# Kernel tuning notes

Measured on AMD Instinct MI355X. Metric: run time of the kernel, lower is better.

The kernel has to match this reference:

```python
import jax, jax.numpy as jnp
import numpy as np

DIM = 256
NH = 4
HD = DIM // NH
RR = 8
EPS_BN = 1e-5


def dwconv(x, w, b):
    # depthwise conv, stride 1, SAME padding (odd kernel, pad=k//2)
    out = jax.lax.conv_general_dilated(
        x, w, window_strides=(1, 1), padding='SAME',
        feature_group_count=x.shape[1],
        dimension_numbers=('NCHW', 'OIHW', 'NCHW'))
    return out + b[None, :, None, None]


def conv1x1(x, w, b):
    # w: [out_c, in_c]
    return jnp.einsum('bchw,oc->bohw', x, w) + b[None, :, None, None]


def bn_eval(x, g, be, m, v):
    inv = g / jnp.sqrt(v + EPS_BN)
    return x * inv[None, :, None, None] + (be - m * inv)[None, :, None, None]


def l2norm(x):
    n = jnp.sqrt(jnp.sum(x * x, axis=-1, keepdims=True))
    return x / jnp.maximum(n, 1e-12)


def setup_inputs() -> dict:
    key = jax.random.key(0)
    ks = jax.random.split(key, 32)
    d = {}
    d['x1'] = jax.random.normal(ks[0], (8, DIM, 64, 64), jnp.float32)
    d['x2'] = jax.random.normal(ks[1], (8, DIM, 64, 64), jnp.float32)
    # multi-scale depthwise convs k=3,5,7
    for i, k in enumerate([3, 5, 7]):
        d[f'ms_w{k}'] = jax.random.normal(ks[2 + i], (DIM, 1, k, k), jnp.float32) * (1.0 / k)
        d[f'ms_b{k}'] = jax.random.normal(ks[5 + i], (DIM,), jnp.float32) * 0.02
    # qkv 1x1 conv + BN params for each stream
    for s, off in [(1, 8), (2, 16)]:
        d[f'qkv{s}_w'] = jax.random.normal(ks[off], (3 * DIM, DIM), jnp.float32) * (DIM ** -0.5)
        d[f'qkv{s}_b'] = jnp.zeros((3 * DIM,), jnp.float32)
        d[f'bn{s}_g'] = 1.0 + 0.1 * jax.random.normal(ks[off + 1], (3 * DIM,), jnp.float32)
        d[f'bn{s}_b'] = 0.1 * jax.random.normal(ks[off + 2], (3 * DIM,), jnp.float32)
        d[f'bn{s}_m'] = 0.1 * jax.random.normal(ks[off + 3], (3 * DIM,), jnp.float32)
        d[f'bn{s}_v'] = jax.random.uniform(ks[off + 4], (3 * DIM,), jnp.float32, 0.5, 1.5)
    # SE channel attention (shared module)
    d['ca_w1'] = jax.random.normal(ks[24], (DIM // RR, DIM), jnp.float32) * (DIM ** -0.5)
    d['ca_b1'] = jnp.zeros((DIM // RR,), jnp.float32)
    d['ca_w2'] = jax.random.normal(ks[25], (DIM, DIM // RR), jnp.float32) * ((DIM // RR) ** -0.5)
    d['ca_b2'] = jnp.zeros((DIM,), jnp.float32)
    # output projections
    d['po1_w'] = jax.random.normal(ks[26], (DIM, DIM), jnp.float32) * (DIM ** -0.5)
    d['po1_b'] = jnp.zeros((DIM,), jnp.float32)
    d['po2_w'] = jax.random.normal(ks[27], (DIM, DIM), jnp.float32) * (DIM ** -0.5)
    d['po2_b'] = jnp.zeros((DIM,), jnp.float32)
    return d


def _scfa(x1, x2, ms_w3, ms_b3, ms_w5, ms_b5, ms_w7, ms_b7,
          qkv1_w, qkv1_b, bn1_g, bn1_b, bn1_m, bn1_v,
          qkv2_w, qkv2_b, bn2_g, bn2_b, bn2_m, bn2_v,
          ca_w1, ca_b1, ca_w2, ca_b2, po1_w, po1_b, po2_w, po2_b):
    b, c, h, w = x1.shape
    temp = HD ** -0.5

    def multi_scale(x):
        return (dwconv(x, ms_w3, ms_b3) + dwconv(x, ms_w5, ms_b5) + dwconv(x, ms_w7, ms_b7)) / 3.0

    x1f = multi_scale(x1)
    x2f = multi_scale(x2)

    qkv1 = jax.nn.gelu(bn_eval(conv1x1(x1f, qkv1_w, qkv1_b), bn1_g, bn1_b, bn1_m, bn1_v), approximate=False)
    qkv2 = jax.nn.gelu(bn_eval(conv1x1(x2f, qkv2_w, qkv2_b), bn2_g, bn2_b, bn2_m, bn2_v), approximate=False)

    def split_heads(t):
        q, k, v = jnp.split(t, 3, axis=1)
        f = lambda z: z.reshape(b, NH, HD, h * w)
        return f(q), f(k), f(v)

    x1_q, x1_k, x1_v = split_heads(qkv1)
    x2_q, x2_k, x2_v = split_heads(qkv2)

    q1, k2 = l2norm(x1_q), l2norm(x2_k)
    q2, k1 = l2norm(x2_q), l2norm(x1_k)

    attn1 = jax.nn.softmax(jnp.einsum('bhcn,bhdn->bhcd', q1, k2) * temp, axis=-1)
    attn2 = jax.nn.softmax(jnp.einsum('bhcn,bhdn->bhcd', q2, k1) * temp, axis=-1)

    x1_out = jnp.einsum('bhcd,bhdn->bhcn', attn1, x1_v).reshape(b, c, h, w)
    x2_out = jnp.einsum('bhcd,bhdn->bhcn', attn2, x2_v).reshape(b, c, h, w)

    def se_gate(x):
        p = x.mean(axis=(2, 3))  # [b, c]
        y = jax.nn.relu(jnp.einsum('bc,rc->br', p, ca_w1) + ca_b1)
        y = jax.nn.sigmoid(jnp.einsum('br,cr->bc', y, ca_w2) + ca_b2)
        return y[:, :, None, None]

    x1_out = x1_out * se_gate(x1_out)
    x2_out = x2_out * se_gate(x2_out)

    x1_out = conv1x1(x1_out, po1_w, po1_b) + x1
    x2_out = conv1x1(x2_out, po2_w, po2_b) + x2
    return x1_out, x2_out


def reference(x1, x2, ms_w3, ms_b3, ms_w5, ms_b5, ms_w7, ms_b7,
              qkv1_w, qkv1_b, bn1_g, bn1_b, bn1_m, bn1_v,
              qkv2_w, qkv2_b, bn2_g, bn2_b, bn2_m, bn2_v,
              ca_w1, ca_b1, ca_w2, ca_b2, po1_w, po1_b, po2_w, po2_b):
    return _scfa(x1, x2, ms_w3, ms_b3, ms_w5, ms_b5, ms_w7, ms_b7,
                 qkv1_w, qkv1_b, bn1_g, bn1_b, bn1_m, bn1_v,
                 qkv2_w, qkv2_b, bn2_g, bn2_b, bn2_m, bn2_v,
                 ca_w1, ca_b1, ca_w2, ca_b2, po1_w, po1_b, po2_w, po2_b)
```

## Files before the change

### kernel.cpp

```cpp
#include <hip/hip_runtime.h>
#include <hip/hip_bf16.h>


#define NPIX 4096

typedef __attribute__((ext_vector_type(8))) short bfrag;
typedef __attribute__((ext_vector_type(4))) float f4acc;

#define GLDS16(g, l) __builtin_amdgcn_global_load_lds( \
    (const __attribute__((address_space(1))) unsigned int*)(g), \
    (__attribute__((address_space(3))) unsigned int*)(l), 16, 0, 0)

__device__ __forceinline__ float bf2f(unsigned short h) {
  return __uint_as_float(((unsigned)h) << 16);
}
__device__ __forceinline__ unsigned short f2bf(float f) {
  unsigned u = __float_as_uint(f);
  unsigned r = (u + 0x7FFFu + ((u >> 16) & 1u)) >> 16;
  return (unsigned short)r;
}
__device__ __forceinline__ float gelu_f(float x) {
  float z = x * (1.5957691216f + 0.0713548163f * x * x);
  return x / (1.0f + __expf(-z));
}

__global__ __launch_bounds__(256) void prep_kernel(
    const float* __restrict__ w3, const float* __restrict__ b3,
    const float* __restrict__ w5, const float* __restrict__ b5,
    const float* __restrict__ w7, const float* __restrict__ b7,
    const float* __restrict__ qb1, const float* __restrict__ g1,
    const float* __restrict__ be1, const float* __restrict__ m1,
    const float* __restrict__ v1,
    const float* __restrict__ qb2, const float* __restrict__ g2,
    const float* __restrict__ be2, const float* __restrict__ m2,
    const float* __restrict__ v2,
    float* __restrict__ weff, float* __restrict__ beff,
    float* __restrict__ alpha, float* __restrict__ beta)
{
  const int c = threadIdx.x;
  for (int ky = 0; ky < 7; ++ky)
    for (int kx = 0; kx < 7; ++kx) {
      float w = w7[c * 49 + ky * 7 + kx];
      if (ky >= 1 && ky <= 5 && kx >= 1 && kx <= 5)
        w += w5[c * 25 + (ky - 1) * 5 + (kx - 1)];
      if (ky >= 2 && ky <= 4 && kx >= 2 && kx <= 4)
        w += w3[c * 9 + (ky - 2) * 3 + (kx - 2)];
      weff[c * 49 + ky * 7 + kx] = w * (1.0f / 3.0f);
    }
  beff[c] = (b3[c] + b5[c] + b7[c]) * (1.0f / 3.0f);
  for (int o = c; o < 768; o += 256) {
    float inv1 = g1[o] / sqrtf(v1[o] + 1e-5f);
    alpha[o] = inv1;
    beta[o]  = qb1[o] * inv1 + be1[o] - m1[o] * inv1;
    float inv2 = g2[o] / sqrtf(v2[o] + 1e-5f);
    alpha[768 + o] = inv2;
    beta[768 + o]  = qb2[o] * inv2 + be2[o] - m2[o] * inv2;
  }
}

__global__ __launch_bounds__(256) void convert_w(
    const float* __restrict__ s1, const float* __restrict__ s2,
    unsigned short* __restrict__ d1, unsigned short* __restrict__ d2)
{
  int idx = blockIdx.x * 256 + threadIdx.x;
  d1[idx] = f2bf(s1[idx]);
  d2[idx] = f2bf(s2[idx]);
}

__global__ __launch_bounds__(256) void ms_conv(
    const float* __restrict__ x1, const float* __restrict__ x2,
    const float* __restrict__ weff, const float* __restrict__ beff,
    unsigned short* __restrict__ xf0, unsigned short* __restrict__ xf1)
{
  __shared__ float tile[5888];
  const int bc2 = blockIdx.x;
  const int s = bc2 >> 11, bc = bc2 & 2047;
  const int c = bc & 255;
  const int tid = threadIdx.x;
  const float* src = (s ? x2 : x1) + (size_t)bc * NPIX;
  float wreg[49];
#pragma unroll
  for (int i = 0; i < 49; ++i) wreg[i] = weff[c * 49 + i];
  const float bias = beff[c];
  float4 vv[4];
#pragma unroll
  for (int k = 0; k < 4; ++k)
    vv[k] = *(const float4*)&src[(k * 256 + tid) * 4];
#pragma unroll
  for (int k = 0; k < 4; ++k) {
    const int idx = k * 256 + tid;
    const int row = (idx >> 4) + 3;
    const int col = 4 + (idx & 15) * 4;
    *(float4*)&tile[84 * row + ((row >> 3) & 1) * 8 + col] = vv[k];
  }
  const float4 zq = {0.0f, 0.0f, 0.0f, 0.0f};
  for (int idx = tid; idx < 306; idx += 256) {
    int row, col;
    if (idx < 114) {
      int r6 = idx / 19;
      col = (idx - r6 * 19) * 4;
      row = (r6 < 3) ? r6 : (r6 + 64);
    } else {
      int j = idx - 114;
      int r64 = j / 3, q = j - r64 * 3;
      row = 3 + r64;
      col = (q == 0) ? 0 : (64 + q * 4);
    }
    *(float4*)&tile[84 * row + ((row >> 3) & 1) * 8 + col] = zq;
  }
  __syncthreads();
  const int x0 = (tid & 15) * 4;
  const int y0 = (tid >> 4) * 4;
  float acc[4][4];
#pragma unroll
  for (int yo = 0; yo < 4; ++yo)
#pragma unroll
    for (int xo = 0; xo < 4; ++xo) acc[yo][xo] = bias;
#pragma unroll
  for (int r = 0; r < 10; ++r) {
    const int row = y0 + r;
    const int rb = 84 * row + ((row >> 3) & 1) * 8 + x0;
    float seg[12];
    *(float4*)&seg[0] = *(const float4*)&tile[rb];
    *(float4*)&seg[4] = *(const float4*)&tile[rb + 4];
    *(float4*)&seg[8] = *(const float4*)&tile[rb + 8];
    const int yolo = (r >= 6) ? (r - 6) : 0;
    const int yohi = (r < 3) ? r : 3;
#pragma unroll
    for (int yo = 0; yo < 4; ++yo) {
      if (yo < yolo || yo > yohi) continue;
      const int ky = r - yo;
#pragma unroll
      for (int kx = 0; kx < 7; ++kx) {
        const float w = wreg[ky * 7 + kx];
#pragma unroll
        for (int xo = 0; xo < 4; ++xo)
          acc[yo][xo] = fmaf(w, seg[1 + xo + kx], acc[yo][xo]);
      }
    }
  }
  unsigned short* dst = (s ? xf1 : xf0) + (size_t)bc * NPIX;
#pragma unroll
  for (int yo = 0; yo < 4; ++yo) {
    ushort4 u;
    u.x = f2bf(acc[yo][0]); u.y = f2bf(acc[yo][1]);
    u.z = f2bf(acc[yo][2]); u.w = f2bf(acc[yo][3]);
    *(ushort4*)&dst[(y0 + yo) * 64 + x0] = u;
  }
}

__global__ __launch_bounds__(256) void transpose_bf16(
    const unsigned short* __restrict__ s0, unsigned short* __restrict__ d0,
    const unsigned short* __restrict__ s1, unsigned short* __restrict__ d1,
    long sb, long db)
{
  __shared__ unsigned short T[64][72];
  const int n0 = blockIdx.x * 64, c0 = blockIdx.y * 64;
  const int z = blockIdx.z, st = z >> 3, b = z & 7;
  const unsigned short* src = st ? s1 : s0;
  unsigned short* dst = st ? d1 : d0;
  const int t = threadIdx.x;
  const int rhi = t >> 4, c4 = (t & 15) * 4;
#pragma unroll
  for (int rr = 0; rr < 4; ++rr) {
    int row = rr * 16 + rhi;
    ushort4 u = *(const ushort4*)&src[(size_t)b * sb + (size_t)(c0 + row) * NPIX + n0 + c4];
    T[row][c4 + 0] = u.x; T[row][c4 + 1] = u.y;
    T[row][c4 + 2] = u.z; T[row][c4 + 3] = u.w;
  }
  __syncthreads();
#pragma unroll
  for (int rr = 0; rr < 4; ++rr) {
    int nrow = rr * 16 + rhi;
    ushort4 u;
    u.x = T[c4 + 0][nrow]; u.y = T[c4 + 1][nrow];
    u.z = T[c4 + 2][nrow]; u.w = T[c4 + 3][nrow];
    *(ushort4*)&dst[(size_t)b * db + (size_t)(n0 + nrow) * 256 + c0 + c4] = u;
  }
}

__global__ __launch_bounds__(256) void qkv_gemm(
    const unsigned short* __restrict__ W1, const unsigned short* __restrict__ W2,
    const unsigned short* __restrict__ X0, const unsigned short* __restrict__ X1,
    const float* __restrict__ alpha, const float* __restrict__ beta,
    unsigned short* __restrict__ q1, unsigned short* __restrict__ q2,
    float* __restrict__ ns)
{
  __shared__ unsigned short As[128 * 64];
  __shared__ unsigned short Bs[256 * 64];
  const int n0 = blockIdx.x * 256, o0 = blockIdx.y * 128;
  const int z = blockIdx.z, s = z >> 3, b = z & 7;
  const unsigned short* Wb = s ? W2 : W1;
  const unsigned short* Xt = s ? X1 : X0;
  unsigned short* qkv = s ? q2 : q1;
  const float* al = alpha + s * 768;
  const float* be = beta + s * 768;
  float* normsq = ns + s * 4096;
  const int tid = threadIdx.x, w = tid >> 6, lane = tid & 63;
  const int wm = (w & 1) * 128;
  const int wn = (w >> 1) * 64;
  const int lrow8 = lane >> 3;
  const int lcolsw = ((lane & 7) ^ lrow8) * 8;
  const int fslot = lane & 7;
  f4acc acc[8][4] = {};
  auto stage = [&](int kc) {
#pragma unroll
    for (int j = 0; j < 4; ++j) {
      int i = w * 4 + j;
      GLDS16(Wb + (size_t)(o0 + i * 8 + lrow8) * 256 + kc + lcolsw, &As[i * 512]);
    }
#pragma unroll
    for (int j = 0; j < 8; ++j) {
      int i = w * 8 + j;
      GLDS16(Xt + (size_t)b * 1048576 + (size_t)(n0 + i * 8 + lrow8) * 256 + kc + lcolsw,
             &Bs[i * 512]);
    }
  };
  stage(0);
#pragma unroll
  for (int t = 0; t < 4; ++t) {
    __syncthreads();
#pragma unroll
    for (int ks = 0; ks < 2; ++ks) {
      const int slot = ((ks * 4 + (lane >> 4)) ^ fslot) * 8;
      bfrag a[8], bb[4];
#pragma unroll
      for (int mt = 0; mt < 8; ++mt)
        a[mt] = *(const bfrag*)&Bs[(wm + mt * 16 + (lane & 15)) * 64 + slot];
#pragma unroll
      for (int nt = 0; nt < 4; ++nt)
        bb[nt] = *(const bfrag*)&As[(wn + nt * 16 + (lane & 15)) * 64 + slot];
#pragma unroll
      for (int mt = 0; mt < 8; ++mt)
#pragma unroll
        for (int nt = 0; nt < 4; ++nt)
          acc[mt][nt] = __builtin_amdgcn_mfma_f32_16x16x32_bf16(a[mt], bb[nt], acc[mt][nt], 0, 0, 0);
    }
    if (t < 3) {
      __syncthreads();
      stage((t + 1) * 64);
    }
  }
#pragma unroll
  for (int nt = 0; nt < 4; ++nt) {
    const int o = o0 + wn + nt * 16 + (lane & 15);
    const float alv = al[o], bev = be[o];
    unsigned short* orow = qkv + ((size_t)b * 768 + o) * NPIX;
    float sq = 0.0f;
#pragma unroll
    for (int mt = 0; mt < 8; ++mt) {
      const int n = n0 + wm + mt * 16 + (lane >> 4) * 4;
      float v0 = gelu_f(acc[mt][nt][0] * alv + bev);
      float v1 = gelu_f(acc[mt][nt][1] * alv + bev);
      float v2 = gelu_f(acc[mt][nt][2] * alv + bev);
      float v3 = gelu_f(acc[mt][nt][3] * alv + bev);
      ushort4 u;
      u.x = f2bf(v0); u.y = f2bf(v1); u.z = f2bf(v2); u.w = f2bf(v3);
      *(ushort4*)&orow[n] = u;
      sq += v0 * v0 + v1 * v1 + v2 * v2 + v3 * v3;
    }
    if (o0 + wn + nt * 16 < 512) {
      sq += __shfl_xor(sq, 16);
      sq += __shfl_xor(sq, 32);
      if (lane < 16) atomicAdd(&normsq[b * 512 + o], sq);
    }
  }
}

__global__ __launch_bounds__(256) void spart_kernel(
    const unsigned short* __restrict__ qkv1, const unsigned short* __restrict__ qkv2,
    float* __restrict__ Sp0, float* __restrict__ Sp1)
{
  __shared__ unsigned short Qs[2][64 * 128];
  __shared__ unsigned short Ks[2][64 * 128];
  const int ck = blockIdx.x, h = blockIdx.y;
  const int z = blockIdx.z, s = z >> 3, b = z & 7;
  const unsigned short* qs = s ? qkv2 : qkv1;
  const unsigned short* kp = (s ? qkv1 : qkv2) + 256 * NPIX;
  float* Sp = s ? Sp1 : Sp0;
  const int tid = threadIdx.x, w = tid >> 6, lane = tid & 63;
  const int lrow16 = lane >> 4;
  const size_t qbase = ((size_t)b * 768 + h * 64) * NPIX;
  f4acc acc[4] = {};
  auto stage = [&](int buf, int it) {
    const int noff = ck * 512 + it * 128;
#pragma unroll
    for (int j = 0; j < 4; ++j) {
      int i = w * 4 + j;
      int row = i * 4 + lrow16;
      int colsw = ((lane & 15) ^ (row & 15)) * 8;
      GLDS16(qs + qbase + (size_t)row * NPIX + noff + colsw, &Qs[buf][i * 512]);
      GLDS16(kp + qbase + (size_t)row * NPIX + noff + colsw, &Ks[buf][i * 512]);
    }
  };
  stage(0, 0);
#pragma unroll
  for (int it = 0; it < 4; ++it) {
    const int cur = it & 1;
    if (it < 3) stage(cur ^ 1, it + 1);
    if (it < 3) asm volatile("s_waitcnt vmcnt(8)" ::: "memory");
    else        asm volatile("s_waitcnt vmcnt(0)" ::: "memory");
    __builtin_amdgcn_s_barrier();
#pragma unroll
    for (int kk = 0; kk < 4; ++kk) {
      const int slot = ((kk * 4 + (lane >> 4)) ^ (lane & 15)) * 8;
      bfrag bq = *(const bfrag*)&Qs[cur][(w * 16 + (lane & 15)) * 128 + slot];
#pragma unroll
      for (int mt = 0; mt < 4; ++mt) {
        bfrag ak = *(const bfrag*)&Ks[cur][(mt * 16 + (lane & 15)) * 128 + slot];
        acc[mt] = __builtin_amdgcn_mfma_f32_16x16x32_bf16(ak, bq, acc[mt], 0, 0, 0);
      }
    }
    __builtin_amdgcn_s_barrier();
  }
  float* dst = Sp + ((size_t)(ck * 32) + b * 4 + h) * 4096;
  const int c = w * 16 + (lane & 15);
#pragma unroll
  for (int mt = 0; mt < 4; ++mt)
    *(float4*)&dst[c * 64 + mt * 16 + (lane >> 4) * 4] = *(float4*)&acc[mt];
}

__global__ __launch_bounds__(256) void softattn(
    const float* __restrict__ Sp0, const float* __restrict__ Sp1,
    const float* __restrict__ ns,
    unsigned short* __restrict__ at0, unsigned short* __restrict__ at1)
{
  const int bh2 = blockIdx.x;
  const int s = bh2 >> 5, bh = bh2 & 31;
  const int b = bh >> 2, h = bh & 3;
  const float* Sp = s ? Sp1 : Sp0;
  const float* nsq = ns + s * 4096;
  const float* nsk = ns + (s ^ 1) * 4096;
  unsigned short* attn = s ? at1 : at0;
  const int wv = threadIdx.x >> 6, lane = threadIdx.x & 63;
  const float ikd = 1.0f / fmaxf(sqrtf(nsk[b * 512 + 256 + h * 64 + lane]), 1e-12f);
  for (int c = wv; c < 64; c += 4) {
    float sm = 0.0f;
#pragma unroll
    for (int ch = 0; ch < 8; ++ch)
      sm += Sp[((size_t)(ch * 32) + bh) * 4096 + c * 64 + lane];
    const float iq = 1.0f / fmaxf(sqrtf(nsq[b * 512 + h * 64 + c]), 1e-12f);
    float zv = sm * 0.125f * iq * ikd;
    float m = zv;
#pragma unroll
    for (int off = 32; off > 0; off >>= 1) m = fmaxf(m, __shfl_xor(m, off));
    float e = expf(zv - m);
    float sum = e;
#pragma unroll
    for (int off = 32; off > 0; off >>= 1) sum += __shfl_xor(sum, off);
    attn[(size_t)bh * 4096 + c * 64 + lane] = f2bf(e / sum);
  }
}

__global__ __launch_bounds__(256) void av_kernel(
    const unsigned short* __restrict__ vt0, const unsigned short* __restrict__ vt1,
    const unsigned short* __restrict__ at0, const unsigned short* __restrict__ at1,
    unsigned short* __restrict__ xo0, unsigned short* __restrict__ xo1,
    long db, float* __restrict__ pool)
{
  __shared__ unsigned short Vs[256 * 64];
  __shared__ unsigned short At[64 * 64];
  const int n0 = blockIdx.x * 256, h = blockIdx.y;
  const int z = blockIdx.z, s = z >> 3, b = z & 7;
  const unsigned short* vt = s ? vt1 : vt0;
  const unsigned short* attn = s ? at1 : at0;
  unsigned short* xout = s ? xo1 : xo0;
  float* pl = pool + s * 2048;
  const int tid = threadIdx.x, w = tid >> 6, lane = tid & 63;
  const int lrow8 = lane >> 3;
  const int lcolsw = ((lane & 7) ^ lrow8) * 8;
  const int bh = b * 4 + h;
#pragma unroll
  for (int j = 0; j < 8; ++j) {
    int i = w * 8 + j;
    GLDS16(vt + ((size_t)b * 1048576 + (size_t)(n0 + i * 8 + lrow8) * 256) + h * 64 + lcolsw,
           &Vs[i * 512]);
  }
#pragma unroll
  for (int j = 0; j < 2; ++j) {
    int i = w * 2 + j;
    GLDS16(attn + (size_t)bh * 4096 + (size_t)(i * 8 + lrow8) * 64 + lcolsw, &At[i * 512]);
  }
  __syncthreads();
  f4acc acc[4][4] = {};
#pragma unroll
  for (int ks = 0; ks < 2; ++ks) {
    const int slot = ((ks * 4 + (lane >> 4)) ^ (lane & 7)) * 8;
    bfrag a[4], bb[4];
#pragma unroll
    for (int mt = 0; mt < 4; ++mt)
      a[mt] = *(const bfrag*)&At[(mt * 16 + (lane & 15)) * 64 + slot];
#pragma unroll
    for (int nt = 0; nt < 4; ++nt)
      bb[nt] = *(const bfrag*)&Vs[(w * 64 + nt * 16 + (lane & 15)) * 64 + slot];
#pragma unroll
    for (int mt = 0; mt < 4; ++mt)
#pragma unroll
      for (int nt = 0; nt < 4; ++nt)
        acc[mt][nt] = __builtin_amdgcn_mfma_f32_16x16x32_bf16(a[mt], bb[nt], acc[mt][nt], 0, 0, 0);
  }
#pragma unroll
  for (int mt = 0; mt < 4; ++mt) {
    const int c = mt * 16 + (lane >> 4) * 4;
    float s0 = 0.0f, s1 = 0.0f, s2 = 0.0f, s3 = 0.0f;
#pragma unroll
    for (int nt = 0; nt < 4; ++nt) {
      const int np = n0 + w * 64 + nt * 16 + (lane & 15);
      ushort4 u;
      u.x = f2bf(acc[mt][nt][0]); u.y = f2bf(acc[mt][nt][1]);
      u.z = f2bf(acc[mt][nt][2]); u.w = f2bf(acc[mt][nt][3]);
      *(ushort4*)&xout[(size_t)b * db + (size_t)np * 256 + h * 64 + c] = u;
      s0 += acc[mt][nt][0]; s1 += acc[mt][nt][1];
      s2 += acc[mt][nt][2]; s3 += acc[mt][nt][3];
    }
    s0 += __shfl_xor(s0, 1); s0 += __shfl_xor(s0, 2); s0 += __shfl_xor(s0, 4); s0 += __shfl_xor(s0, 8);
    s1 += __shfl_xor(s1, 1); s1 += __shfl_xor(s1, 2); s1 += __shfl_xor(s1, 4); s1 += __shfl_xor(s1, 8);
    s2 += __shfl_xor(s2, 1); s2 += __shfl_xor(s2, 2); s2 += __shfl_xor(s2, 4); s2 += __shfl_xor(s2, 8);
    s3 += __shfl_xor(s3, 1); s3 += __shfl_xor(s3, 2); s3 += __shfl_xor(s3, 4); s3 += __shfl_xor(s3, 8);
    if ((lane & 15) == 0) {
      atomicAdd(&pl[b * 256 + h * 64 + c + 0], s0);
      atomicAdd(&pl[b * 256 + h * 64 + c + 1], s1);
      atomicAdd(&pl[b * 256 + h * 64 + c + 2], s2);
      atomicAdd(&pl[b * 256 + h * 64 + c + 3], s3);
    }
  }
}

__global__ __launch_bounds__(256) void segate_scale(
    const float* __restrict__ pool, const float* __restrict__ w1,
    const float* __restrict__ b1, const float* __restrict__ w2,
    const float* __restrict__ b2,
    const float* __restrict__ W1, const float* __restrict__ W2,
    unsigned short* __restrict__ Wg)
{
  const int b16 = blockIdx.x;
  const int tid = threadIdx.x;
  __shared__ float p[256];
  __shared__ float hh[32];
  p[tid] = pool[b16 * 256 + tid] * (1.0f / 4096.0f);
  __syncthreads();
  if (tid < 32) {
    float s = b1[tid];
    for (int c = 0; c < 256; ++c) s = fmaf(w1[tid * 256 + c], p[c], s);
    hh[tid] = fmaxf(s, 0.0f);
  }
  __syncthreads();
  float s = b2[tid];
#pragma unroll
  for (int r = 0; r < 32; ++r) s = fmaf(w2[tid * 32 + r], hh[r], s);
  const float g = 1.0f / (1.0f + expf(-s));
  const float* W = (b16 >> 3) ? W2 : W1;
  for (int o = 0; o < 256; ++o)
    Wg[(size_t)b16 * 65536 + o * 256 + tid] = f2bf(W[o * 256 + tid] * g);
}

__global__ __launch_bounds__(256) void pout_gemm(
    const unsigned short* __restrict__ Wgall,
    const unsigned short* __restrict__ X0, const unsigned short* __restrict__ X1,
    long db, const float* __restrict__ bias0, const float* __restrict__ bias1,
    const float* __restrict__ xr0, const float* __restrict__ xr1,
    float* __restrict__ out)
{
  __shared__ unsigned short As[2][128 * 64];
  __shared__ unsigned short Bs[2][128 * 64];
  const int n0 = blockIdx.x * 128, o0 = blockIdx.y * 128;
  const int z = blockIdx.z, s = z >> 3, b = z & 7;
  const unsigned short* Wg = Wgall + (size_t)z * 65536;
  const unsigned short* Xt = s ? X1 : X0;
  const float* bias = s ? bias1 : bias0;
  const float* xresb = s ? xr1 : xr0;
  float* outb = out + (size_t)s * 8388608;
  const int tid = threadIdx.x, w = tid >> 6, lane = tid & 63;
  const int wm = (w & 1) * 64;
  const int wn = (w >> 1) * 64;
  const int lrow8 = lane >> 3;
  const int lcolsw = ((lane & 7) ^ lrow8) * 8;
  const int fslot = lane & 7;
  f4acc acc[4][4] = {};
  auto stage = [&](int buf, int kc) {
#pragma unroll
    for (int j = 0; j < 4; ++j) {
      int i = w * 4 + j;
      GLDS16(Wg + (size_t)(o0 + i * 8 + lrow8) * 256 + kc + lcolsw, &As[buf][i * 512]);
      GLDS16(Xt + (size_t)b * db + (size_t)(n0 + i * 8 + lrow8) * 256 + kc + lcolsw,
             &Bs[buf][i * 512]);
    }
  };
  stage(0, 0);
#pragma unroll
  for (int t = 0; t < 4; ++t) {
    const int cur = t & 1;
    if (t < 3) stage(cur ^ 1, (t + 1) * 64);
    if (t < 3) asm volatile("s_waitcnt vmcnt(8)" ::: "memory");
    else       asm volatile("s_waitcnt vmcnt(0)" ::: "memory");
    __builtin_amdgcn_s_barrier();
#pragma unroll
    for (int ks = 0; ks < 2; ++ks) {
      const int slot = ((ks * 4 + (lane >> 4)) ^ fslot) * 8;
      bfrag a[4], bb[4];
#pragma unroll
      for (int mt = 0; mt < 4; ++mt)
        a[mt] = *(const bfrag*)&Bs[cur][(wm + mt * 16 + (lane & 15)) * 64 + slot];
#pragma unroll
      for (int nt = 0; nt < 4; ++nt)
        bb[nt] = *(const bfrag*)&As[cur][(wn + nt * 16 + (lane & 15)) * 64 + slot];
#pragma unroll
      for (int mt = 0; mt < 4; ++mt)
#pragma unroll
        for (int nt = 0; nt < 4; ++nt)
          acc[mt][nt] = __builtin_amdgcn_mfma_f32_16x16x32_bf16(a[mt], bb[nt], acc[mt][nt], 0, 0, 0);
    }
    __builtin_amdgcn_s_barrier();
  }
#pragma unroll
  for (int nt = 0; nt < 4; ++nt) {
    const int o = o0 + wn + nt * 16 + (lane & 15);
    const float bi = bias[o];
    const float* res = xresb + ((size_t)b * 256 + o) * NPIX;
    float* orow = outb + ((size_t)b * 256 + o) * NPIX;
#pragma unroll
    for (int mt = 0; mt < 4; ++mt) {
      const int n = n0 + wm + mt * 16 + (lane >> 4) * 4;
      float4 r4 = *(const float4*)&res[n];
      float4 ov;
      ov.x = acc[mt][nt][0] + bi + r4.x;
      ov.y = acc[mt][nt][1] + bi + r4.y;
      ov.z = acc[mt][nt][2] + bi + r4.z;
      ov.w = acc[mt][nt][3] + bi + r4.w;
      *(float4*)&orow[n] = ov;
    }
  }
}

extern "C" void kernel_launch(void* const* d_in, const int* in_sizes, int n_in,
                              void* d_out, int out_size, void* d_ws, size_t ws_size,
                              hipStream_t stream) {
  const float* x1    = (const float*)d_in[0];
  const float* x2    = (const float*)d_in[1];
  const float* ms_w3 = (const float*)d_in[2];
  const float* ms_b3 = (const float*)d_in[3];
  const float* ms_w5 = (const float*)d_in[4];
  const float* ms_b5 = (const float*)d_in[5];
  const float* ms_w7 = (const float*)d_in[6];
  const float* ms_b7 = (const float*)d_in[7];
  const float* qkv1_w = (const float*)d_in[8];
  const float* qkv1_b = (const float*)d_in[9];
  const float* bn1_g = (const float*)d_in[10];
  const float* bn1_b = (const float*)d_in[11];
  const float* bn1_m = (const float*)d_in[12];
  const float* bn1_v = (const float*)d_in[13];
  const float* qkv2_w = (const float*)d_in[14];
  const float* qkv2_b = (const float*)d_in[15];
  const float* bn2_g = (const float*)d_in[16];
  const float* bn2_b = (const float*)d_in[17];
  const float* bn2_m = (const float*)d_in[18];
  const float* bn2_v = (const float*)d_in[19];
  const float* ca_w1 = (const float*)d_in[20];
  const float* ca_b1 = (const float*)d_in[21];
  const float* ca_w2 = (const float*)d_in[22];
  const float* ca_b2 = (const float*)d_in[23];
  const float* po1_w = (const float*)d_in[24];
  const float* po1_b = (const float*)d_in[25];
  const float* po2_w = (const float*)d_in[26];
  const float* po2_b = (const float*)d_in[27];

  char* ws = (char*)d_ws;
  float* weff  = (float*)(ws + 0);
  float* beff  = (float*)(ws + 51200);
  float* alpha = (float*)(ws + 53248);
  float* beta  = (float*)(ws + 59392);
  float* normsq = (float*)(ws + 65536);
  float* pool  = (float*)(ws + 98304);
  unsigned short* W1b = (unsigned short*)(ws + 131072);
  unsigned short* W2b = (unsigned short*)(ws + 524288);
  unsigned short* Wg  = (unsigned short*)(ws + 917504);
  unsigned short* attn1 = (unsigned short*)(ws + 3014656);
  unsigned short* attn2 = (unsigned short*)(ws + 3276800);
  float* Sp    = (float*)(ws + 3538944);
  unsigned short* xf   = (unsigned short*)(ws + 7733248);
  unsigned short* xf_t = (unsigned short*)(ws + 24510464);
  unsigned short* qkv1 = (unsigned short*)(ws + 41287680);
  unsigned short* qkv2 = (unsigned short*)(ws + 91619328);
  unsigned short* xf2   = (unsigned short*)d_out;
  unsigned short* xf2_t = (unsigned short*)((char*)d_out + 16777216);
  float* Sp2 = (float*)(ws + 7733248);
  unsigned short* v1t   = xf;
  unsigned short* v2t   = xf_t;
  unsigned short* xout1 = qkv2;
  unsigned short* xout2 = qkv1;
  const long QKV_BSTR = 768L * 4096;

  float* outf = (float*)d_out;

  prep_kernel<<<1, 256, 0, stream>>>(ms_w3, ms_b3, ms_w5, ms_b5, ms_w7, ms_b7,
                                     qkv1_b, bn1_g, bn1_b, bn1_m, bn1_v,
                                     qkv2_b, bn2_g, bn2_b, bn2_m, bn2_v,
                                     weff, beff, alpha, beta);
  convert_w<<<768, 256, 0, stream>>>(qkv1_w, qkv2_w, W1b, W2b);
  hipMemsetAsync(ws + 65536, 0, 49152, stream);

  ms_conv<<<4096, 256, 0, stream>>>(x1, x2, weff, beff, xf, xf2);
  transpose_bf16<<<dim3(64, 4, 16), 256, 0, stream>>>(xf, xf_t, xf2, xf2_t,
                                                      1048576L, 1048576L);
  qkv_gemm<<<dim3(16, 6, 16), 256, 0, stream>>>(W1b, W2b, xf_t, xf2_t,
                                                alpha, beta, qkv1, qkv2, normsq);

  spart_kernel<<<dim3(8, 4, 16), 256, 0, stream>>>(qkv1, qkv2, Sp, Sp2);
  softattn<<<64, 256, 0, stream>>>(Sp, Sp2, normsq, attn1, attn2);

  transpose_bf16<<<dim3(64, 4, 16), 256, 0, stream>>>(qkv1 + 512 * NPIX, v1t,
                                                      qkv2 + 512 * NPIX, v2t,
                                                      3145728L, 1048576L);

  av_kernel<<<dim3(16, 4, 16), 256, 0, stream>>>(v1t, v2t, attn1, attn2,
                                                 xout1, xout2, QKV_BSTR, pool);

  segate_scale<<<16, 256, 0, stream>>>(pool, ca_w1, ca_b1, ca_w2, ca_b2,
                                       po1_w, po2_w, Wg);

  pout_gemm<<<dim3(32, 2, 16), 256, 0, stream>>>(Wg, xout1, xout2, QKV_BSTR,
                                                 po1_b, po2_b, x1, x2, outf);
}
```

Measured before the change: 401.3 us.

## Fuse V transpose into QKV GEMM epilogue and halve GEMM N-tile

The QKV GEMM blocks that produce V now stage their GELU outputs through shared memory and write V directly in transposed (pixel-major) layout. This removes the separate transpose_bf16 launch and its read and rewrite of the V slices. The GEMM N-tile drops from 256 to 128 pixels, which doubles the grid and lowers accumulator register use, at the cost of less reuse per block. The GELU division is replaced with a hardware reciprocal, and the V-transposed buffers move into unused space in the output buffer.

```diff
diff --git a/kernel.cpp b/kernel.cpp
--- a/kernel.cpp
+++ b/kernel.cpp
@@ -21,7 +21,7 @@
 }
 __device__ __forceinline__ float gelu_f(float x) {
   float z = x * (1.5957691216f + 0.0713548163f * x * x);
-  return x / (1.0f + __expf(-z));
+  return x * __builtin_amdgcn_rcpf(1.0f + __expf(-z));
 }
 
 __global__ __launch_bounds__(256) void prep_kernel(
@@ -184,11 +184,13 @@
     const unsigned short* __restrict__ X0, const unsigned short* __restrict__ X1,
     const float* __restrict__ alpha, const float* __restrict__ beta,
     unsigned short* __restrict__ q1, unsigned short* __restrict__ q2,
-    float* __restrict__ ns)
-{
-  __shared__ unsigned short As[128 * 64];
-  __shared__ unsigned short Bs[256 * 64];
-  const int n0 = blockIdx.x * 256, o0 = blockIdx.y * 128;
+    float* __restrict__ ns,
+    unsigned short* __restrict__ v1t, unsigned short* __restrict__ v2t)
+{
+  __shared__ unsigned short smem[16384];
+  unsigned short* As = smem;
+  unsigned short* Bs = smem + 8192;
+  const int n0 = blockIdx.x * 128, o0 = blockIdx.y * 128;
   const int z = blockIdx.z, s = z >> 3, b = z & 7;
   const unsigned short* Wb = s ? W2 : W1;
   const unsigned short* Xt = s ? X1 : X0;
@@ -196,22 +198,19 @@
   const float* al = alpha + s * 768;
   const float* be = beta + s * 768;
   float* normsq = ns + s * 4096;
+  const bool vsw = (o0 >= 512);
   const int tid = threadIdx.x, w = tid >> 6, lane = tid & 63;
-  const int wm = (w & 1) * 128;
+  const int wm = (w & 1) * 64;
   const int wn = (w >> 1) * 64;
   const int lrow8 = lane >> 3;
   const int lcolsw = ((lane & 7) ^ lrow8) * 8;
   const int fslot = lane & 7;
-  f4acc acc[8][4] = {};
+  f4acc acc[4][4] = {};
   auto stage = [&](int kc) {
 #pragma unroll
     for (int j = 0; j < 4; ++j) {
       int i = w * 4 + j;
       GLDS16(Wb + (size_t)(o0 + i * 8 + lrow8) * 256 + kc + lcolsw, &As[i * 512]);
-    }
-#pragma unroll
-    for (int j = 0; j < 8; ++j) {
-      int i = w * 8 + j;
       GLDS16(Xt + (size_t)b * 1048576 + (size_t)(n0 + i * 8 + lrow8) * 256 + kc + lcolsw,
              &Bs[i * 512]);
     }
@@ -223,15 +222,15 @@
 #pragma unroll
     for (int ks = 0; ks < 2; ++ks) {
       const int slot = ((ks * 4 + (lane >> 4)) ^ fslot) * 8;
-      bfrag a[8], bb[4];
-#pragma unroll
-      for (int mt = 0; mt < 8; ++mt)
+      bfrag a[4], bb[4];
+#pragma unroll
+      for (int mt = 0; mt < 4; ++mt)
         a[mt] = *(const bfrag*)&Bs[(wm + mt * 16 + (lane & 15)) * 64 + slot];
 #pragma unroll
       for (int nt = 0; nt < 4; ++nt)
         bb[nt] = *(const bfrag*)&As[(wn + nt * 16 + (lane & 15)) * 64 + slot];
 #pragma unroll
-      for (int mt = 0; mt < 8; ++mt)
+      for (int mt = 0; mt < 4; ++mt)
 #pragma unroll
         for (int nt = 0; nt < 4; ++nt)
           acc[mt][nt] = __builtin_amdgcn_mfma_f32_16x16x32_bf16(a[mt], bb[nt], acc[mt][nt], 0, 0, 0);
@@ -241,28 +240,58 @@
       stage((t + 1) * 64);
     }
   }
-#pragma unroll
-  for (int nt = 0; nt < 4; ++nt) {
-    const int o = o0 + wn + nt * 16 + (lane & 15);
-    const float alv = al[o], bev = be[o];
-    unsigned short* orow = qkv + ((size_t)b * 768 + o) * NPIX;
-    float sq = 0.0f;
-#pragma unroll
-    for (int mt = 0; mt < 8; ++mt) {
-      const int n = n0 + wm + mt * 16 + (lane >> 4) * 4;
-      float v0 = gelu_f(acc[mt][nt][0] * alv + bev);
-      float v1 = gelu_f(acc[mt][nt][1] * alv + bev);
-      float v2 = gelu_f(acc[mt][nt][2] * alv + bev);
-      float v3 = gelu_f(acc[mt][nt][3] * alv + bev);
-      ushort4 u;
-      u.x = f2bf(v0); u.y = f2bf(v1); u.z = f2bf(v2); u.w = f2bf(v3);
-      *(ushort4*)&orow[n] = u;
-      sq += v0 * v0 + v1 * v1 + v2 * v2 + v3 * v3;
-    }
-    if (o0 + wn + nt * 16 < 512) {
+  if (!vsw) {
+#pragma unroll
+    for (int nt = 0; nt < 4; ++nt) {
+      const int o = o0 + wn + nt * 16 + (lane & 15);
+      const float alv = al[o], bev = be[o];
+      unsigned short* orow = qkv + ((size_t)b * 768 + o) * NPIX;
+      float sq = 0.0f;
+#pragma unroll
+      for (int mt = 0; mt < 4; ++mt) {
+        const int n = n0 + wm + mt * 16 + (lane >> 4) * 4;
+        float v0 = gelu_f(acc[mt][nt][0] * alv + bev);
+        float v1 = gelu_f(acc[mt][nt][1] * alv + bev);
+        float v2 = gelu_f(acc[mt][nt][2] * alv + bev);
+        float v3 = gelu_f(acc[mt][nt][3] * alv + bev);
+        ushort4 u;
+        u.x = f2bf(v0); u.y = f2bf(v1); u.z = f2bf(v2); u.w = f2bf(v3);
+        *(ushort4*)&orow[n] = u;
+        sq += v0 * v0 + v1 * v1 + v2 * v2 + v3 * v3;
+      }
       sq += __shfl_xor(sq, 16);
       sq += __shfl_xor(sq, 32);
       if (lane < 16) atomicAdd(&normsq[b * 512 + o], sq);
+    }
+  } else {
+    __syncthreads();
+#pragma unroll
+    for (int nt = 0; nt < 4; ++nt) {
+      const int o = o0 + wn + nt * 16 + (lane & 15);
+      const float alv = al[o], bev = be[o];
+      const int ol = wn + nt * 16 + (lane & 15);
+#pragma unroll
+      for (int mt = 0; mt < 4; ++mt) {
+        const int nb = wm + mt * 16 + (lane >> 4) * 4;
+#pragma unroll
+        for (int j = 0; j < 4; ++j) {
+          const int nl = nb + j;
+          smem[(nl * 128 + ol) ^ (((nl >> 2) & 7) << 3)] =
+              f2bf(gelu_f(acc[mt][nt][j] * alv + bev));
+        }
+      }
+    }
+    __syncthreads();
+    unsigned short* vtb = (s ? v2t : v1t) + (size_t)b * 1048576;
+    const int row = tid & 127;
+    const int cg = (tid >> 7) * 8;
+    const int c0 = o0 - 512;
+#pragma unroll
+    for (int ch = 0; ch < 8; ++ch) {
+      const int chunk = cg + ch;
+      const int idx = (row * 128 + chunk * 8) ^ (((row >> 2) & 7) << 3);
+      float4 v4 = *(const float4*)&smem[idx];
+      *(float4*)&vtb[(size_t)(n0 + row) * 256 + c0 + chunk * 8] = v4;
     }
   }
 }
@@ -583,9 +612,9 @@
   unsigned short* qkv2 = (unsigned short*)(ws + 91619328);
   unsigned short* xf2   = (unsigned short*)d_out;
   unsigned short* xf2_t = (unsigned short*)((char*)d_out + 16777216);
+  unsigned short* v2t   = (unsigned short*)((char*)d_out + 33554432);
+  unsigned short* v1t   = (unsigned short*)((char*)d_out + 50331648);
   float* Sp2 = (float*)(ws + 7733248);
-  unsigned short* v1t   = xf;
-  unsigned short* v2t   = xf_t;
   unsigned short* xout1 = qkv2;
   unsigned short* xout2 = qkv1;
   const long QKV_BSTR = 768L * 4096;
@@ -602,16 +631,13 @@
   ms_conv<<<4096, 256, 0, stream>>>(x1, x2, weff, beff, xf, xf2);
   transpose_bf16<<<dim3(64, 4, 16), 256, 0, stream>>>(xf, xf_t, xf2, xf2_t,
                                                       1048576L, 1048576L);
-  qkv_gemm<<<dim3(16, 6, 16), 256, 0, stream>>>(W1b, W2b, xf_t, xf2_t,
-                                                alpha, beta, qkv1, qkv2, normsq);
+  qkv_gemm<<<dim3(32, 6, 16), 256, 0, stream>>>(W1b, W2b, xf_t, xf2_t,
+                                                alpha, beta, qkv1, qkv2, normsq,
+                                                v1t, v2t);
 
   spart_kernel<<<dim3(8, 4, 16), 256, 0, stream>>>(qkv1, qkv2, Sp, Sp2);
   softattn<<<64, 256, 0, stream>>>(Sp, Sp2, normsq, attn1, attn2);
 
-  transpose_bf16<<<dim3(64, 4, 16), 256, 0, stream>>>(qkv1 + 512 * NPIX, v1t,
-                                                      qkv2 + 512 * NPIX, v2t,
-                                                      3145728L, 1048576L);
-
   av_kernel<<<dim3(16, 4, 16), 256, 0, stream>>>(v1t, v2t, attn1, attn2,
                                                  xout1, xout2, QKV_BSTR, pool);
 
```

Result: faster. 372.0 us (-7.3%).
